# Kernel optimization log

Hardware: AMD Instinct MI355X
Metric: run time of the kernel (lower is better)

Reference implementation:

```python
import jax, jax.numpy as jnp
import numpy as np

N_NODES = 100000
N_EDGES = 1600000
NUM_FEATURES = 64
HIDDEN = 64
NUM_CLASSES = 16


def setup_inputs() -> dict:
    key = jax.random.key(0)
    ks = jax.random.split(key, 8)
    x = jax.random.normal(ks[0], (N_NODES, NUM_FEATURES), dtype=jnp.float32)
    edge_index = jax.random.randint(ks[1], (2, N_EDGES), 0, N_NODES, dtype=jnp.int32)
    # Glorot-ish init for weights, zero bias (matches GCNConv / Linear defaults closely enough)
    s1 = 1.0 / np.sqrt(NUM_FEATURES)
    s2 = 1.0 / np.sqrt(HIDDEN)
    W1 = jax.random.uniform(ks[2], (NUM_FEATURES, HIDDEN), jnp.float32, -s1, s1)
    b1 = jnp.zeros((HIDDEN,), jnp.float32)
    W2 = jax.random.uniform(ks[3], (HIDDEN, HIDDEN), jnp.float32, -s2, s2)
    b2 = jnp.zeros((HIDDEN,), jnp.float32)
    W3 = jax.random.uniform(ks[4], (HIDDEN, NUM_CLASSES), jnp.float32, -s2, s2)
    b3 = jax.random.uniform(ks[5], (NUM_CLASSES,), jnp.float32, -s2, s2)
    return {"x": x, "edge_index": edge_index, "W1": W1, "b1": b1,
            "W2": W2, "b2": b2, "W3": W3, "b3": b3}


def _gcn_layer(x, W, b, src, dst, norm, n_nodes):
    # GCNConv: h = X W; out[i] = sum_{(j->i)} norm_ji * h[j]; out += b
    h = x @ W                                   # [N, H] small dense GEMM
    msg = h[src] * norm[:, None]                # [E+N, H] irregular gather
    out = jax.ops.segment_sum(msg, dst, num_segments=n_nodes)  # scatter-add
    return out + b


def reference(x, edge_index, W1, b1, W2, b2, W3, b3):
    n = x.shape[0]
    loop = jnp.arange(n, dtype=edge_index.dtype)
    # add self-loops (PyG GCNConv default add_self_loops=True)
    src = jnp.concatenate([edge_index[0], loop])
    dst = jnp.concatenate([edge_index[1], loop])
    # symmetric normalization D^{-1/2} A_hat D^{-1/2}
    deg = jax.ops.segment_sum(jnp.ones_like(src, dtype=x.dtype), dst, num_segments=n)
    dis = jax.lax.rsqrt(deg)                    # deg >= 1 due to self-loops
    norm = dis[src] * dis[dst]                  # [E+N]

    h = jax.nn.relu(_gcn_layer(x, W1, b1, src, dst, norm, n))
    # F.dropout(training=False) -> identity (module in eval mode)
    h = jax.nn.relu(_gcn_layer(h, W2, b2, src, dst, norm, n))
    z = h @ W3 + b3
    return jax.nn.log_softmax(z, axis=1), h
```

## Files before the change

kernel.cpp:

```cpp
#include <hip/hip_runtime.h>
#include <hip/hip_bf16.h>

typedef __hip_bfloat16 bf16;
typedef unsigned short ushort;

#define NN 100000
#define NE 1600000
#define NBKT 391
#define BCAP 4608
#define EPB 4096
#define NP1 391
#define NMT 6250

typedef __attribute__((ext_vector_type(8))) short s8v;
typedef __attribute__((ext_vector_type(4))) float f4v;
typedef __attribute__((ext_vector_type(2))) float f2v;

__device__ __forceinline__ float ldf(const void* p, int i, int f32) {
    return f32 ? ((const float*)p)[i] : __bfloat162float(((const bf16*)p)[i]);
}
__device__ __forceinline__ void stf(void* p, int i, int f32, float v) {
    if (f32) ((float*)p)[i] = v;
    else     ((bf16*)p)[i] = __float2bfloat16(v);
}

__device__ __forceinline__ ushort f2b(float f) {
    unsigned u = __builtin_bit_cast(unsigned, f);
    u += 0x7FFF + ((u >> 16) & 1);
    return (ushort)(u >> 16);
}
__device__ __forceinline__ float b2f(ushort h) {
    unsigned u = ((unsigned)h) << 16;
    return __builtin_bit_cast(float, u);
}
__device__ __forceinline__ float blo(unsigned u) {
    return __builtin_bit_cast(float, u << 16);
}
__device__ __forceinline__ float bhi(unsigned u) {
    return __builtin_bit_cast(float, u & 0xffff0000u);
}
__device__ __forceinline__ f2v up2(unsigned u) {
    f2v r; r.x = blo(u); r.y = bhi(u); return r;
}

__global__ void k_sentinel(unsigned* out) {
    if (threadIdx.x == 0 && blockIdx.x == 0) out[0] = 0x461C461Cu;
}

__global__ void k_cnt(const unsigned* __restrict__ x, int* __restrict__ flag,
                      const int* __restrict__ dst, int* __restrict__ cnt) {
    __shared__ int hist[NBKT];
    int b = blockIdx.x, t = threadIdx.x;
    for (int i = t; i < NBKT; i += 256) hist[i] = 0;
    __syncthreads();
    int e0 = b * EPB;
#pragma unroll
    for (int k = 0; k < EPB; k += 256) {
        int e = e0 + k + t;
        if (e < NE) atomicAdd(&hist[dst[e] >> 8], 1);
    }
    __syncthreads();
    for (int i = t; i < NBKT; i += 256) cnt[b * NBKT + i] = hist[i];
    if (b == 0) {
        int c = 0;
        for (int i = t; i < 2048; i += 256) {
            unsigned e7 = (x[i] >> 8) & 0x7F;
            c += (e7 >= 60 && e7 <= 66) ? 1 : 0;
        }
        __syncthreads();
        hist[t] = c;
        __syncthreads();
        for (int s = 128; s > 0; s >>= 1) {
            if (t < s) hist[t] += hist[t + s];
            __syncthreads();
        }
        if (t == 0) *flag = (hist[0] >= 1024) ? 0 : 1;
    }
}

__global__ void k_colscan(const int* __restrict__ cnt, int* __restrict__ prefT,
                          int* __restrict__ btot) {
    __shared__ int s[512];
    int k = blockIdx.x, t = threadIdx.x;
    int v = (t < NP1) ? cnt[t * NBKT + k] : 0;
    s[t] = v;
    __syncthreads();
    for (int d = 1; d < 512; d <<= 1) {
        int add = (t >= d) ? s[t - d] : 0;
        __syncthreads();
        s[t] += add;
        __syncthreads();
    }
    if (t < NP1) prefT[k * NP1 + t] = s[t] - v;
    if (t == 511) btot[k] = s[511];
}

__global__ void k_place(const int* __restrict__ src, const int* __restrict__ dst,
                        const int* __restrict__ prefT, unsigned* __restrict__ bbuf) {
    __shared__ int base[NBKT];
    __shared__ int lcur[NBKT];
    int b = blockIdx.x, t = threadIdx.x;
    for (int i = t; i < NBKT; i += 256) {
        base[i] = prefT[i * NP1 + b];
        lcur[i] = 0;
    }
    __syncthreads();
    int e0 = b * EPB;
#pragma unroll
    for (int k = 0; k < EPB; k += 256) {
        int e = e0 + k + t;
        if (e < NE) {
            int d = dst[e];
            int kb = d >> 8;
            int lp = atomicAdd(&lcur[kb], 1);
            bbuf[kb * BCAP + base[kb] + lp] = ((unsigned)src[e] << 8) | (unsigned)(d & 255);
        }
    }
}

__global__ void k_pass2(const unsigned* __restrict__ bbuf, const int* __restrict__ btot,
                        int* __restrict__ rowptr, float* __restrict__ dis,
                        int* __restrict__ csr_off) {
    __shared__ unsigned vals[BCAP];
    __shared__ int lout[BCAP];
    __shared__ int fh[256], fx[256], fc[256];
    int b = blockIdx.x, t = threadIdx.x;
    int part = 0;
    for (int i = t; i < b; i += 256) part += btot[i];
    fh[t] = part;
    __syncthreads();
    for (int s = 128; s > 0; s >>= 1) {
        if (t < s) fh[t] += fh[t + s];
        __syncthreads();
    }
    int g0 = fh[0];
    int cntb = btot[b];
    if (b == 0 && t == 0) rowptr[NN] = NE;
    __syncthreads();
    const unsigned* in = bbuf + b * BCAP;
    fh[t] = 0;
    __syncthreads();
    for (int i = t; i < cntb; i += 256) {
        unsigned v = in[i];
        vals[i] = v;
        atomicAdd(&fh[v & 255], 1);
    }
    __syncthreads();
    fx[t] = fh[t];
    __syncthreads();
    for (int d = 1; d < 256; d <<= 1) {
        int add = (t >= d) ? fx[t - d] : 0;
        __syncthreads();
        fx[t] += add;
        __syncthreads();
    }
    int n = b * 256 + t;
    int ex = fx[t] - fh[t];
    fc[t] = ex;
    if (n < NN) {
        rowptr[n] = g0 + ex;
        dis[n] = rsqrtf(1.0f + (float)fh[t]);
    }
    __syncthreads();
    for (int i = t; i < cntb; i += 256) {
        unsigned v = vals[i];
        int p = atomicAdd(&fc[v & 255], 1);
        lout[p] = (int)((v >> 8) << 7);
    }
    __syncthreads();
    for (int i = t; i < cntb; i += 256) csr_off[g0 + i] = lout[i];
}

__global__ void __launch_bounds__(256) k_gemm_mfma(
        const void* __restrict__ A, int aBase, const void* __restrict__ W,
        bf16* __restrict__ C, const float* __restrict__ dis,
        const int* __restrict__ flag) {
    int f32 = *flag;
    int t = threadIdx.x;
    if (blockIdx.x == 0 && t < 64) ((ushort*)C)[NN * 64 + t] = 0;
    int lane = t & 63;
    int w = t >> 6;
    int m = lane & 15, q = lane >> 4;

    s8v bh[2][4], bl[2][4];
#pragma unroll
    for (int st = 0; st < 2; st++)
#pragma unroll
        for (int nt = 0; nt < 4; nt++)
#pragma unroll
            for (int j = 0; j < 8; j++) {
                int k = st * 32 + q * 8 + j;
                float wv = ldf(W, k * 64 + nt * 16 + m, f32);
                ushort h = f2b(wv);
                bh[st][nt][j] = (short)h;
                bl[st][nt][j] = (short)f2b(wv - b2f(h));
            }

    ushort* Cu = (ushort*)C;
    int gw = blockIdx.x * 4 + w;
    int nw = gridDim.x * 4;
    for (int mt = gw; mt < NMT; mt += nw) {
        int row = mt * 16 + m;
        s8v ah[2], al[2];
        if (f32) {
            const float* ap = (const float*)A + aBase + row * 64 + q * 8;
#pragma unroll
            for (int st = 0; st < 2; st++)
#pragma unroll
                for (int j = 0; j < 8; j++) {
                    float v = ap[st * 32 + j];
                    ushort h = f2b(v);
                    ah[st][j] = (short)h;
                    al[st][j] = (short)f2b(v - b2f(h));
                }
        } else {
            const short* ap = (const short*)A + aBase + row * 64 + q * 8;
            ah[0] = *(const s8v*)(ap);
            ah[1] = *(const s8v*)(ap + 32);
        }
        float dr[4];
#pragma unroll
        for (int r = 0; r < 4; r++) dr[r] = dis[mt * 16 + q * 4 + r];
#pragma unroll
        for (int nt = 0; nt < 4; nt++) {
            f4v acc = {0.f, 0.f, 0.f, 0.f};
#pragma unroll
            for (int st = 0; st < 2; st++)
                acc = __builtin_amdgcn_mfma_f32_16x16x32_bf16(ah[st], bh[st][nt], acc, 0, 0, 0);
            if (f32) {
#pragma unroll
                for (int st = 0; st < 2; st++) {
                    acc = __builtin_amdgcn_mfma_f32_16x16x32_bf16(ah[st], bl[st][nt], acc, 0, 0, 0);
                    acc = __builtin_amdgcn_mfma_f32_16x16x32_bf16(al[st], bh[st][nt], acc, 0, 0, 0);
                }
            }
            int col = nt * 16 + m;
#pragma unroll
            for (int r = 0; r < 4; r++) {
                int rr = mt * 16 + q * 4 + r;
                Cu[rr * 64 + col] = f2b(dr[r] * acc[r]);
            }
        }
    }
}

template<int MODE>
__global__ void __launch_bounds__(256, 8) k_aggregate(
        const bf16* __restrict__ hs, void* hout, int hoBase,
        const float* __restrict__ dis,
        const int* __restrict__ rowptr,
        const int* __restrict__ csr_off,
        const void* __restrict__ bias,
        const int* __restrict__ flag,
        const void* __restrict__ W3, const void* __restrict__ b3,
        void* __restrict__ lgout) {
    int f32 = *flag;
    int t = threadIdx.x;
    int l = t & 63;
    int q = l >> 4;
    int m = l & 15;
    int fb = m * 8;
    const char* hb = (const char*)hs;
    float b0 = ldf(bias, m * 4 + 0, f32);
    float b1v = ldf(bias, m * 4 + 1, f32);
    float b2v = ldf(bias, m * 4 + 2, f32);
    float b3v = ldf(bias, m * 4 + 3, f32);
    float hb3[4];
    float w3r[4][4];
    if constexpr (MODE == 1) {
#pragma unroll
        for (int i = 0; i < 4; i++)
#pragma unroll
            for (int j2 = 0; j2 < 4; j2++)
                w3r[i][j2] = ldf(W3, (m * 4 + i) * 16 + q * 4 + j2, f32);
#pragma unroll
        for (int j2 = 0; j2 < 4; j2++) hb3[j2] = ldf(b3, q * 4 + j2, f32);
    }
    const int Z = NN * 128;
    int wid = blockIdx.x * 4 + (t >> 6);
    int nwav = gridDim.x * 4;
    for (int n = wid; n < NN; n += nwav) {
        int r0 = rowptr[n], r1 = rowptr[n + 1];
        f2v a01 = {0.f, 0.f}, a23 = {0.f, 0.f};
        int j = r0;
        for (; j + 16 <= r1; j += 16) {
            int o0 = csr_off[j + q];
            int o1 = csr_off[j + 4 + q];
            int o2 = csr_off[j + 8 + q];
            int o3 = csr_off[j + 12 + q];
            uint2 v0 = *(const uint2*)(hb + o0 + fb);
            uint2 v1 = *(const uint2*)(hb + o1 + fb);
            uint2 v2 = *(const uint2*)(hb + o2 + fb);
            uint2 v3 = *(const uint2*)(hb + o3 + fb);
            a01 += up2(v0.x); a23 += up2(v0.y);
            a01 += up2(v1.x); a23 += up2(v1.y);
            a01 += up2(v2.x); a23 += up2(v2.y);
            a01 += up2(v3.x); a23 += up2(v3.y);
        }
        if (j < r1) {
            int i0 = j + q, i1 = j + 4 + q, i2 = j + 8 + q, i3 = j + 12 + q;
            int o0 = csr_off[i0]; o0 = (i0 < r1) ? o0 : Z;
            int o1 = csr_off[i1]; o1 = (i1 < r1) ? o1 : Z;
            int o2 = csr_off[i2]; o2 = (i2 < r1) ? o2 : Z;
            int o3 = csr_off[i3]; o3 = (i3 < r1) ? o3 : Z;
            uint2 v0 = *(const uint2*)(hb + o0 + fb);
            uint2 v1 = *(const uint2*)(hb + o1 + fb);
            uint2 v2 = *(const uint2*)(hb + o2 + fb);
            uint2 v3 = *(const uint2*)(hb + o3 + fb);
            a01 += up2(v0.x); a23 += up2(v0.y);
            a01 += up2(v1.x); a23 += up2(v1.y);
            a01 += up2(v2.x); a23 += up2(v2.y);
            a01 += up2(v3.x); a23 += up2(v3.y);
        }
        float a0 = a01.x, a1 = a01.y, a2 = a23.x, a3 = a23.y;
        a0 += __shfl_xor(a0, 32); a1 += __shfl_xor(a1, 32);
        a2 += __shfl_xor(a2, 32); a3 += __shfl_xor(a3, 32);
        a0 += __shfl_xor(a0, 16); a1 += __shfl_xor(a1, 16);
        a2 += __shfl_xor(a2, 16); a3 += __shfl_xor(a3, 16);
        if constexpr (MODE == 0) {
            if (q == 0) {
                uint2 sv = *(const uint2*)(hb + n * 128 + fb);
                float dn = dis[n];
                float o0 = fmaxf(dn * (a0 + blo(sv.x)) + b0, 0.f);
                float o1 = fmaxf(dn * (a1 + bhi(sv.x)) + b1v, 0.f);
                float o2 = fmaxf(dn * (a2 + blo(sv.y)) + b2v, 0.f);
                float o3 = fmaxf(dn * (a3 + bhi(sv.y)) + b3v, 0.f);
                if (f32) {
                    float4 ov = {o0, o1, o2, o3};
                    *(float4*)((float*)hout + hoBase + n * 64 + m * 4) = ov;
                } else {
                    unsigned w0 = (unsigned)f2b(o0) | ((unsigned)f2b(o1) << 16);
                    unsigned w1 = (unsigned)f2b(o2) | ((unsigned)f2b(o3) << 16);
                    uint2 wv; wv.x = w0; wv.y = w1;
                    *(uint2*)((ushort*)hout + hoBase + n * 64 + m * 4) = wv;
                }
            }
        } else {
            uint2 sv = *(const uint2*)(hb + n * 128 + fb);
            float dn = dis[n];
            float o0 = fmaxf(dn * (a0 + blo(sv.x)) + b0, 0.f);
            float o1 = fmaxf(dn * (a1 + bhi(sv.x)) + b1v, 0.f);
            float o2 = fmaxf(dn * (a2 + blo(sv.y)) + b2v, 0.f);
            float o3 = fmaxf(dn * (a3 + bhi(sv.y)) + b3v, 0.f);
            if (q == 0) {
                if (f32) {
                    float4 ov = {o0, o1, o2, o3};
                    *(float4*)((float*)hout + hoBase + n * 64 + m * 4) = ov;
                } else {
                    unsigned w0 = (unsigned)f2b(o0) | ((unsigned)f2b(o1) << 16);
                    unsigned w1 = (unsigned)f2b(o2) | ((unsigned)f2b(o3) << 16);
                    uint2 wv; wv.x = w0; wv.y = w1;
                    *(uint2*)((ushort*)hout + hoBase + n * 64 + m * 4) = wv;
                }
            }
            float z0, z1, z2, z3;
            z0 = o0 * w3r[0][0]; z1 = o0 * w3r[0][1];
            z2 = o0 * w3r[0][2]; z3 = o0 * w3r[0][3];
            z0 += o1 * w3r[1][0]; z1 += o1 * w3r[1][1];
            z2 += o1 * w3r[1][2]; z3 += o1 * w3r[1][3];
            z0 += o2 * w3r[2][0]; z1 += o2 * w3r[2][1];
            z2 += o2 * w3r[2][2]; z3 += o2 * w3r[2][3];
            z0 += o3 * w3r[3][0]; z1 += o3 * w3r[3][1];
            z2 += o3 * w3r[3][2]; z3 += o3 * w3r[3][3];
#pragma unroll
            for (int msk = 1; msk <= 8; msk <<= 1) {
                z0 += __shfl_xor(z0, msk); z1 += __shfl_xor(z1, msk);
                z2 += __shfl_xor(z2, msk); z3 += __shfl_xor(z3, msk);
            }
            z0 += hb3[0]; z1 += hb3[1]; z2 += hb3[2]; z3 += hb3[3];
            float M = fmaxf(fmaxf(z0, z1), fmaxf(z2, z3));
            M = fmaxf(M, __shfl_xor(M, 16));
            M = fmaxf(M, __shfl_xor(M, 32));
            float es = __expf(z0 - M) + __expf(z1 - M)
                     + __expf(z2 - M) + __expf(z3 - M);
            es += __shfl_xor(es, 16);
            es += __shfl_xor(es, 32);
            float ls = __logf(es) + M;
            if (m == 0) {
                if (f32) {
                    float4 ov = {z0 - ls, z1 - ls, z2 - ls, z3 - ls};
                    *(float4*)((float*)lgout + n * 16 + q * 4) = ov;
                } else {
                    unsigned p0 = (unsigned)f2b(z0 - ls) | ((unsigned)f2b(z1 - ls) << 16);
                    unsigned p1 = (unsigned)f2b(z2 - ls) | ((unsigned)f2b(z3 - ls) << 16);
                    uint2 pv; pv.x = p0; pv.y = p1;
                    *(uint2*)((ushort*)lgout + n * 16 + q * 4) = pv;
                }
            }
        }
    }
}

extern "C" void kernel_launch(void* const* d_in, const int* in_sizes, int n_in,
                              void* d_out, int out_size, void* d_ws, size_t ws_size,
                              hipStream_t stream) {
    const void* x  = d_in[0];
    const int* ei  = (const int*)d_in[1];
    const void* W1 = d_in[2];
    const void* b1 = d_in[3];
    const void* W2 = d_in[4];
    const void* b2 = d_in[5];
    const void* W3 = d_in[6];
    const void* b3 = d_in[7];

    const size_t NEEDED = (size_t)(1807104 + 3203072) * 4;
    if (ws_size < NEEDED) {
        k_sentinel<<<1, 64, 0, stream>>>((unsigned*)d_out);
        return;
    }
    int*      flag    = (int*)d_ws;
    float*    dis     = (float*)d_ws + 256;
    int*      rowptr  = (int*)d_ws + 102656;
    int*      btot    = (int*)d_ws + 205568;
    int*      csr_off = (int*)d_ws + 207104;
    unsigned* bbuf    = (unsigned*)((int*)d_ws + 1807104);
    int*      cnt     = (int*)d_ws + 1807104 + NBKT * BCAP;
    int*      prefT   = cnt + 153088;
    bf16*     bufA    = (bf16*)bbuf;

    const int* srcp = ei;
    const int* dstp = ei + NE;
    const int HB = NN * 16;

    k_cnt<<<NP1, 256, 0, stream>>>((const unsigned*)x, flag, dstp, cnt);
    k_colscan<<<NBKT, 512, 0, stream>>>(cnt, prefT, btot);
    k_place<<<NP1, 256, 0, stream>>>(srcp, dstp, prefT, bbuf);
    k_pass2<<<NBKT, 256, 0, stream>>>(bbuf, btot, rowptr, dis, csr_off);

    k_gemm_mfma<<<512, 256, 0, stream>>>(x, 0, W1, bufA, dis, flag);
    k_aggregate<0><<<2048, 256, 0, stream>>>(bufA, d_out, HB, dis, rowptr,
                                             csr_off, b1, flag,
                                             nullptr, nullptr, nullptr);

    k_gemm_mfma<<<512, 256, 0, stream>>>(d_out, HB, W2, bufA, dis, flag);
    k_aggregate<1><<<2048, 256, 0, stream>>>(bufA, d_out, HB, dis, rowptr,
                                             csr_off, b2, flag,
                                             W3, b3, d_out);
}
```

Before: 257.7 us.

## Stage bucket placement in LDS, vectorize GEMM loads, move W3 to shared

k_place now runs with 512 threads. Each block builds a local histogram of its edges per bucket, prefix-scans it, and sorts its edges by bucket in LDS before writing them out, so the global stores to bbuf land in contiguous runs instead of being scattered one by one. The fp32 GEMM path reads its A operand with 128-bit vector loads instead of scalar loads. The final-layer aggregate keeps W3 in padded shared memory rather than in 16 registers per thread, which should lower register pressure. The costs are extra LDS use and barriers in k_place, and float4 reads from a stride-17 padded LDS array that may be misaligned.

```diff
diff --git a/kernel.cpp b/kernel.cpp
--- a/kernel.cpp
+++ b/kernel.cpp
@@ -95,27 +95,62 @@
     if (t == 511) btot[k] = s[511];
 }
 
-__global__ void k_place(const int* __restrict__ src, const int* __restrict__ dst,
-                        const int* __restrict__ prefT, unsigned* __restrict__ bbuf) {
+__global__ void __launch_bounds__(512) k_place(
+        const int* __restrict__ src, const int* __restrict__ dst,
+        const int* __restrict__ prefT, unsigned* __restrict__ bbuf) {
     __shared__ int base[NBKT];
-    __shared__ int lcur[NBKT];
+    __shared__ int hist[NBKT];
+    __shared__ int lofs[512];
+    __shared__ unsigned vals[EPB];
+    __shared__ int addr[EPB];
     int b = blockIdx.x, t = threadIdx.x;
-    for (int i = t; i < NBKT; i += 256) {
+    for (int i = t; i < NBKT; i += 512) {
         base[i] = prefT[i * NP1 + b];
-        lcur[i] = 0;
+        hist[i] = 0;
     }
     __syncthreads();
     int e0 = b * EPB;
-#pragma unroll
-    for (int k = 0; k < EPB; k += 256) {
-        int e = e0 + k + t;
+    unsigned ev[8];
+    int kb[8];
+#pragma unroll
+    for (int k = 0; k < 8; k++) {
+        int e = e0 + k * 512 + t;
         if (e < NE) {
             int d = dst[e];
-            int kb = d >> 8;
-            int lp = atomicAdd(&lcur[kb], 1);
-            bbuf[kb * BCAP + base[kb] + lp] = ((unsigned)src[e] << 8) | (unsigned)(d & 255);
-        }
-    }
+            ev[k] = ((unsigned)src[e] << 8) | (unsigned)(d & 255);
+            kb[k] = d >> 8;
+        } else kb[k] = -1;
+    }
+#pragma unroll
+    for (int k = 0; k < 8; k++)
+        if (kb[k] >= 0) atomicAdd(&hist[kb[k]], 1);
+    __syncthreads();
+    int v = (t < NBKT) ? hist[t] : 0;
+    lofs[t] = v;
+    __syncthreads();
+    for (int d = 1; d < 512; d <<= 1) {
+        int add = (t >= d) ? lofs[t - d] : 0;
+        __syncthreads();
+        lofs[t] += add;
+        __syncthreads();
+    }
+    int ex = lofs[t] - v;
+    __syncthreads();
+    lofs[t] = ex;
+    if (t < NBKT) hist[t] = 0;
+    __syncthreads();
+#pragma unroll
+    for (int k = 0; k < 8; k++) {
+        if (kb[k] >= 0) {
+            int p = atomicAdd(&hist[kb[k]], 1);
+            int li = lofs[kb[k]] + p;
+            vals[li] = ev[k];
+            addr[li] = kb[k] * BCAP + base[kb[k]] + p;
+        }
+    }
+    __syncthreads();
+    int tot = min(EPB, NE - e0);
+    for (int i = t; i < tot; i += 512) bbuf[addr[i]] = vals[i];
 }
 
 __global__ void k_pass2(const unsigned* __restrict__ bbuf, const int* __restrict__ btot,
@@ -205,14 +240,17 @@
         if (f32) {
             const float* ap = (const float*)A + aBase + row * 64 + q * 8;
 #pragma unroll
-            for (int st = 0; st < 2; st++)
+            for (int st = 0; st < 2; st++) {
+                f4v va = *(const f4v*)(ap + st * 32);
+                f4v vb = *(const f4v*)(ap + st * 32 + 4);
 #pragma unroll
                 for (int j = 0; j < 8; j++) {
-                    float v = ap[st * 32 + j];
+                    float v = (j < 4) ? va[j] : vb[j - 4];
                     ushort h = f2b(v);
                     ah[st][j] = (short)h;
                     al[st][j] = (short)f2b(v - b2f(h));
                 }
+            }
         } else {
             const short* ap = (const short*)A + aBase + row * 64 + q * 8;
             ah[0] = *(const s8v*)(ap);
@@ -254,6 +292,7 @@
         const int* __restrict__ flag,
         const void* __restrict__ W3, const void* __restrict__ b3,
         void* __restrict__ lgout) {
+    __shared__ float w3s[MODE ? 64 * 17 : 1];
     int f32 = *flag;
     int t = threadIdx.x;
     int l = t & 63;
@@ -266,15 +305,12 @@
     float b2v = ldf(bias, m * 4 + 2, f32);
     float b3v = ldf(bias, m * 4 + 3, f32);
     float hb3[4];
-    float w3r[4][4];
     if constexpr (MODE == 1) {
-#pragma unroll
-        for (int i = 0; i < 4; i++)
-#pragma unroll
-            for (int j2 = 0; j2 < 4; j2++)
-                w3r[i][j2] = ldf(W3, (m * 4 + i) * 16 + q * 4 + j2, f32);
+        for (int i = t; i < 1024; i += 256)
+            w3s[(i >> 4) * 17 + (i & 15)] = ldf(W3, i, f32);
 #pragma unroll
         for (int j2 = 0; j2 < 4; j2++) hb3[j2] = ldf(b3, q * 4 + j2, f32);
+        __syncthreads();
     }
     const int Z = NN * 128;
     int wid = blockIdx.x * 4 + (t >> 6);
@@ -353,15 +389,14 @@
                     *(uint2*)((ushort*)hout + hoBase + n * 64 + m * 4) = wv;
                 }
             }
-            float z0, z1, z2, z3;
-            z0 = o0 * w3r[0][0]; z1 = o0 * w3r[0][1];
-            z2 = o0 * w3r[0][2]; z3 = o0 * w3r[0][3];
-            z0 += o1 * w3r[1][0]; z1 += o1 * w3r[1][1];
-            z2 += o1 * w3r[1][2]; z3 += o1 * w3r[1][3];
-            z0 += o2 * w3r[2][0]; z1 += o2 * w3r[2][1];
-            z2 += o2 * w3r[2][2]; z3 += o2 * w3r[2][3];
-            z0 += o3 * w3r[3][0]; z1 += o3 * w3r[3][1];
-            z2 += o3 * w3r[3][2]; z3 += o3 * w3r[3][3];
+            float z0 = 0.f, z1 = 0.f, z2 = 0.f, z3 = 0.f;
+            float oo[4] = {o0, o1, o2, o3};
+#pragma unroll
+            for (int i = 0; i < 4; i++) {
+                float4 wv = *(const float4*)(w3s + (m * 4 + i) * 17 + q * 4);
+                z0 += oo[i] * wv.x; z1 += oo[i] * wv.y;
+                z2 += oo[i] * wv.z; z3 += oo[i] * wv.w;
+            }
 #pragma unroll
             for (int msk = 1; msk <= 8; msk <<= 1) {
                 z0 += __shfl_xor(z0, msk); z1 += __shfl_xor(z1, msk);
@@ -424,7 +459,7 @@
 
     k_cnt<<<NP1, 256, 0, stream>>>((const unsigned*)x, flag, dstp, cnt);
     k_colscan<<<NBKT, 512, 0, stream>>>(cnt, prefT, btot);
-    k_place<<<NP1, 256, 0, stream>>>(srcp, dstp, prefT, bbuf);
+    k_place<<<NP1, 512, 0, stream>>>(srcp, dstp, prefT, bbuf);
     k_pass2<<<NBKT, 256, 0, stream>>>(bbuf, btot, rowptr, dis, csr_off);
 
     k_gemm_mfma<<<512, 256, 0, stream>>>(x, 0, W1, bufA, dis, flag);
```

After: 241.4 us. -6.3%, faster.
